# Kernel tuning notes

Measured on AMD Instinct MI355X. Metric: run time of the kernel, lower is better.

The kernel has to match this reference:

```python
import jax, jax.numpy as jnp
import numpy as np

EPS = 1e-6

def _feature(x):
    # phi(x) = concat(relu(x), relu(-x)) along the last dim: (b,h,n,d) -> (b,h,n,2d)
    return jnp.concatenate([jax.nn.relu(x), jax.nn.relu(-x)], axis=-1)

def setup_inputs() -> dict:
    key = jax.random.key(0)
    kq, kk, kv = jax.random.split(key, 3)
    shape = (4, 16, 8192, 64)  # (batch, heads, seq_len, dim)
    Q = jax.random.normal(kq, shape, dtype=jnp.float32)
    K = jax.random.normal(kk, shape, dtype=jnp.float32)
    V = jax.random.normal(kv, shape, dtype=jnp.float32)
    return {"Q": Q, "K": K, "V": V}

def reference(Q, K, V):
    Qf = _feature(Q)  # (b,h,n,2d)
    Kf = _feature(K)  # (b,h,n,2d)
    # KV outer-product reduction over sequence: (b,h,2d,m)
    KV = jnp.einsum('bhnd,bhnm->bhdm', Kf, V)
    out = jnp.einsum('bhnd,bhdm->bhnm', Qf, KV)  # (b,h,n,m)
    K_sum = Kf.sum(axis=2)  # (b,h,2d)
    normalizer = jnp.einsum('bhnd,bhd->bhn', Qf, K_sum)  # (b,h,n)
    return out / (normalizer[..., None] + EPS)
```

## Files before the change

kernel.cpp:

```cpp
#include <hip/hip_runtime.h>

typedef __bf16 bf16x8 __attribute__((ext_vector_type(8)));
typedef __bf16 bf16x4 __attribute__((ext_vector_type(4)));
typedef float f32x4 __attribute__((ext_vector_type(4)));

#define BH_TOT 64
#define SEQ 8192
#define DIM 64
#define NCH 16
#define CHN (SEQ / NCH)
#define KV_STRIDE 68
#define KV_ROWS 128

__global__ __launch_bounds__(256) void fla_ph1(const float* __restrict__ K,
                                               const float* __restrict__ V,
                                               float* __restrict__ kvf) {
  const int blk = blockIdx.x;
  const int bh = blk / NCH;
  const int ch = blk % NCH;
  const float* Kp = K + (size_t)bh * SEQ * DIM + (size_t)ch * CHN * DIM;
  const float* Vp = V + (size_t)bh * SEQ * DIM + (size_t)ch * CHN * DIM;

  __shared__ __bf16 Kb[32][68];
  __shared__ __bf16 Vb[32][68];

  const int tid = threadIdx.x;
  const int lane = tid & 63;
  const int w = tid >> 6;
  const int quad = lane >> 4;
  const int col = lane & 15;

  f32x4 acc[2][5];
#pragma unroll
  for (int mt = 0; mt < 2; ++mt)
#pragma unroll
    for (int nt = 0; nt < 5; ++nt)
      acc[mt][nt] = (f32x4){0.f, 0.f, 0.f, 0.f};

  bf16x8 bones;
#pragma unroll
  for (int j = 0; j < 8; ++j) bones[j] = (__bf16)0.f;
  if (col == 0) {
#pragma unroll
    for (int j = 0; j < 8; ++j) bones[j] = (__bf16)1.0f;
  }

  const int fcol0 = ((w & 1) << 5) + col;
  const bool neg = (w >= 2);

  for (int s = 0; s < CHN / 32; ++s) {
    const float* Ks = Kp + s * 32 * DIM;
    const float* Vs = Vp + s * 32 * DIM;
    __syncthreads();
#pragma unroll
    for (int i = 0; i < 2; ++i) {
      int idx = tid + i * 256;
      int r = idx >> 4;
      int c4 = (idx & 15) << 2;
      float4 kk = *(const float4*)(Ks + r * DIM + c4);
      float4 vv = *(const float4*)(Vs + r * DIM + c4);
      bf16x4 kb4, vb4;
      kb4[0] = (__bf16)kk.x; kb4[1] = (__bf16)kk.y;
      kb4[2] = (__bf16)kk.z; kb4[3] = (__bf16)kk.w;
      vb4[0] = (__bf16)vv.x; vb4[1] = (__bf16)vv.y;
      vb4[2] = (__bf16)vv.z; vb4[3] = (__bf16)vv.w;
      *(bf16x4*)&Kb[r][c4] = kb4;
      *(bf16x4*)&Vb[r][c4] = vb4;
    }
    __syncthreads();

    bf16x8 a0, a1, bfr[5];
#pragma unroll
    for (int j = 0; j < 8; ++j) {
      int rr = quad * 8 + j;
      float k0 = (float)Kb[rr][fcol0];
      float k1 = (float)Kb[rr][fcol0 + 16];
      if (neg) { k0 = -k0; k1 = -k1; }
      a0[j] = (__bf16)fmaxf(k0, 0.f);
      a1[j] = (__bf16)fmaxf(k1, 0.f);
      bfr[0][j] = Vb[rr][col];
      bfr[1][j] = Vb[rr][col + 16];
      bfr[2][j] = Vb[rr][col + 32];
      bfr[3][j] = Vb[rr][col + 48];
    }
    bfr[4] = bones;
#pragma unroll
    for (int nt = 0; nt < 5; ++nt) {
      acc[0][nt] = __builtin_amdgcn_mfma_f32_16x16x32_bf16(a0, bfr[nt], acc[0][nt], 0, 0, 0);
      acc[1][nt] = __builtin_amdgcn_mfma_f32_16x16x32_bf16(a1, bfr[nt], acc[1][nt], 0, 0, 0);
    }
  }

  float* dst = kvf + (size_t)bh * KV_ROWS * KV_STRIDE;
#pragma unroll
  for (int mt = 0; mt < 2; ++mt) {
    int feat = (w * 2 + mt) * 16 + quad * 4;
#pragma unroll
    for (int nt = 0; nt < 5; ++nt) {
      int c = nt * 16 + col;
      if (c <= 64) {
#pragma unroll
        for (int r = 0; r < 4; ++r)
          atomicAdd(&dst[(size_t)(feat + r) * KV_STRIDE + c], acc[mt][nt][r]);
      }
    }
  }
}

__global__ __launch_bounds__(256) void fla_ph2(const float* __restrict__ Q,
                                               const float* __restrict__ kvf,
                                               float* __restrict__ out) {
  const int blk = blockIdx.x;
  const int bh = blk >> 5;
  const int rb = blk & 31;
  const float* Qp = Q + (size_t)bh * SEQ * DIM + (size_t)rb * 256 * DIM;
  float* Op = out + (size_t)bh * SEQ * DIM + (size_t)rb * 256 * DIM;

  __shared__ __bf16 kvb[128][66];
  const float* src = kvf + (size_t)bh * KV_ROWS * KV_STRIDE;
  for (int i = threadIdx.x; i < 128 * 66; i += 256) {
    int k = i / 66;
    int c = i - k * 66;
    float v = (c <= 64) ? src[(size_t)k * KV_STRIDE + c] : 0.f;
    kvb[k][c] = (__bf16)v;
  }
  __syncthreads();

  const int lane = threadIdx.x & 63;
  const int w = threadIdx.x >> 6;
  const int quad = lane >> 4;
  const int col = lane & 15;

  bf16x8 bfr[4][5];
#pragma unroll
  for (int kt = 0; kt < 4; ++kt) {
#pragma unroll
    for (int j = 0; j < 8; ++j) {
      int k = kt * 32 + quad * 8 + j;
      bfr[kt][0][j] = kvb[k][col];
      bfr[kt][1][j] = kvb[k][col + 16];
      bfr[kt][2][j] = kvb[k][col + 32];
      bfr[kt][3][j] = kvb[k][col + 48];
      bfr[kt][4][j] = (col == 0) ? kvb[k][64] : (__bf16)0.f;
    }
  }

#pragma unroll
  for (int mt = 0; mt < 4; ++mt) {
    const float* qrow = Qp + (size_t)(w * 64 + mt * 16 + col) * DIM;
    float4 q0 = *(const float4*)(qrow + quad * 8);
    float4 q1 = *(const float4*)(qrow + quad * 8 + 4);
    float4 q2 = *(const float4*)(qrow + 32 + quad * 8);
    float4 q3 = *(const float4*)(qrow + 32 + quad * 8 + 4);
    float qv[16];
    *(float4*)&qv[0] = q0;  *(float4*)&qv[4] = q1;
    *(float4*)&qv[8] = q2;  *(float4*)&qv[12] = q3;
    bf16x8 a0, a1, a2, a3;
#pragma unroll
    for (int j = 0; j < 8; ++j) {
      a0[j] = (__bf16)fmaxf(qv[j], 0.f);
      a2[j] = (__bf16)fmaxf(-qv[j], 0.f);
      a1[j] = (__bf16)fmaxf(qv[8 + j], 0.f);
      a3[j] = (__bf16)fmaxf(-qv[8 + j], 0.f);
    }
    f32x4 acc[5];
#pragma unroll
    for (int nt = 0; nt < 5; ++nt) acc[nt] = (f32x4){0.f, 0.f, 0.f, 0.f};
#pragma unroll
    for (int nt = 0; nt < 5; ++nt) {
      acc[nt] = __builtin_amdgcn_mfma_f32_16x16x32_bf16(a0, bfr[0][nt], acc[nt], 0, 0, 0);
      acc[nt] = __builtin_amdgcn_mfma_f32_16x16x32_bf16(a1, bfr[1][nt], acc[nt], 0, 0, 0);
      acc[nt] = __builtin_amdgcn_mfma_f32_16x16x32_bf16(a2, bfr[2][nt], acc[nt], 0, 0, 0);
      acc[nt] = __builtin_amdgcn_mfma_f32_16x16x32_bf16(a3, bfr[3][nt], acc[nt], 0, 0, 0);
    }
    float inv[4];
#pragma unroll
    for (int r = 0; r < 4; ++r) {
      float nrm = __shfl((float)acc[4][r], lane & 48, 64);
      inv[r] = 1.0f / (nrm + 1e-6f);
    }
    float* orow = Op + (size_t)(w * 64 + mt * 16) * DIM;
#pragma unroll
    for (int nt = 0; nt < 4; ++nt)
#pragma unroll
      for (int r = 0; r < 4; ++r)
        orow[(size_t)(quad * 4 + r) * DIM + nt * 16 + col] = acc[nt][r] * inv[r];
  }
}

extern "C" void kernel_launch(void* const* d_in, const int* in_sizes, int n_in,
                              void* d_out, int out_size, void* d_ws, size_t ws_size,
                              hipStream_t stream) {
  const float* Q = (const float*)d_in[0];
  const float* K = (const float*)d_in[1];
  const float* V = (const float*)d_in[2];
  float* out = (float*)d_out;
  float* kvf = (float*)d_ws;

  hipMemsetAsync(kvf, 0, (size_t)BH_TOT * KV_ROWS * KV_STRIDE * sizeof(float), stream);
  fla_ph1<<<dim3(BH_TOT * NCH), dim3(256), 0, stream>>>(K, V, kvf);
  fla_ph2<<<dim3(BH_TOT * 32), dim3(256), 0, stream>>>(Q, kvf, out);
}
```

Measured before the change: 474.8 us.

## Prefetch K/V registers and use 512-thread blocks in phase-one reduction

Phase one now runs 512 threads per block with 8 waves, each owning one 16-feature tile instead of two, and stages 64 rows per iteration. Global loads for the next tile are issued into registers before the LDS store and barrier of the current tile, so memory latency overlaps the MFMA work. The launch bound asks for higher occupancy. In exchange, each wave re-reads V fragments from LDS for both row slices, and the atomic output layout is remapped to the new wave-to-feature assignment.

Result: faster. 457.5 us (-3.7%).

```diff
diff --git a/kernel.cpp b/kernel.cpp
--- a/kernel.cpp
+++ b/kernel.cpp
@@ -9,20 +9,22 @@
 #define DIM 64
 #define NCH 16
 #define CHN (SEQ / NCH)
+#define ROWS 64
+#define NR (CHN / ROWS)
 #define KV_STRIDE 68
 #define KV_ROWS 128
 
-__global__ __launch_bounds__(256) void fla_ph1(const float* __restrict__ K,
-                                               const float* __restrict__ V,
-                                               float* __restrict__ kvf) {
+__global__ __launch_bounds__(512, 8) void fla_ph1(const float* __restrict__ K,
+                                                  const float* __restrict__ V,
+                                                  float* __restrict__ kvf) {
   const int blk = blockIdx.x;
   const int bh = blk / NCH;
   const int ch = blk % NCH;
   const float* Kp = K + (size_t)bh * SEQ * DIM + (size_t)ch * CHN * DIM;
   const float* Vp = V + (size_t)bh * SEQ * DIM + (size_t)ch * CHN * DIM;
 
-  __shared__ __bf16 Kb[32][68];
-  __shared__ __bf16 Vb[32][68];
+  __shared__ __bf16 Kb[ROWS][68];
+  __shared__ __bf16 Vb[ROWS][68];
 
   const int tid = threadIdx.x;
   const int lane = tid & 63;
@@ -30,12 +32,14 @@
   const int quad = lane >> 4;
   const int col = lane & 15;
 
-  f32x4 acc[2][5];
-#pragma unroll
-  for (int mt = 0; mt < 2; ++mt)
-#pragma unroll
-    for (int nt = 0; nt < 5; ++nt)
-      acc[mt][nt] = (f32x4){0.f, 0.f, 0.f, 0.f};
+  const int r0 = tid >> 4;
+  const int c0 = (tid & 15) << 2;
+  const int off0 = r0 * DIM + c0;
+  const int off1 = off0 + 32 * DIM;
+
+  f32x4 acc[5];
+#pragma unroll
+  for (int nt = 0; nt < 5; ++nt) acc[nt] = (f32x4){0.f, 0.f, 0.f, 0.f};
 
   bf16x8 bones;
 #pragma unroll
@@ -45,64 +49,68 @@
     for (int j = 0; j < 8; ++j) bones[j] = (__bf16)1.0f;
   }
 
-  const int fcol0 = ((w & 1) << 5) + col;
-  const bool neg = (w >= 2);
-
-  for (int s = 0; s < CHN / 32; ++s) {
-    const float* Ks = Kp + s * 32 * DIM;
-    const float* Vs = Vp + s * 32 * DIM;
+  const int kcol = ((w & 3) << 4) + col;
+  const bool neg = (w >= 4);
+
+  float4 pk0 = *(const float4*)(Kp + off0);
+  float4 pk1 = *(const float4*)(Kp + off1);
+  float4 pv0 = *(const float4*)(Vp + off0);
+  float4 pv1 = *(const float4*)(Vp + off1);
+
+  for (int s = 0; s < NR; ++s) {
+    bf16x4 kb0, kb1, vb0, vb1;
+    kb0[0] = (__bf16)pk0.x; kb0[1] = (__bf16)pk0.y; kb0[2] = (__bf16)pk0.z; kb0[3] = (__bf16)pk0.w;
+    kb1[0] = (__bf16)pk1.x; kb1[1] = (__bf16)pk1.y; kb1[2] = (__bf16)pk1.z; kb1[3] = (__bf16)pk1.w;
+    vb0[0] = (__bf16)pv0.x; vb0[1] = (__bf16)pv0.y; vb0[2] = (__bf16)pv0.z; vb0[3] = (__bf16)pv0.w;
+    vb1[0] = (__bf16)pv1.x; vb1[1] = (__bf16)pv1.y; vb1[2] = (__bf16)pv1.z; vb1[3] = (__bf16)pv1.w;
+
+    if (s + 1 < NR) {
+      const float* Kn = Kp + (s + 1) * ROWS * DIM;
+      const float* Vn = Vp + (s + 1) * ROWS * DIM;
+      pk0 = *(const float4*)(Kn + off0);
+      pk1 = *(const float4*)(Kn + off1);
+      pv0 = *(const float4*)(Vn + off0);
+      pv1 = *(const float4*)(Vn + off1);
+    }
+
     __syncthreads();
-#pragma unroll
-    for (int i = 0; i < 2; ++i) {
-      int idx = tid + i * 256;
-      int r = idx >> 4;
-      int c4 = (idx & 15) << 2;
-      float4 kk = *(const float4*)(Ks + r * DIM + c4);
-      float4 vv = *(const float4*)(Vs + r * DIM + c4);
-      bf16x4 kb4, vb4;
-      kb4[0] = (__bf16)kk.x; kb4[1] = (__bf16)kk.y;
-      kb4[2] = (__bf16)kk.z; kb4[3] = (__bf16)kk.w;
-      vb4[0] = (__bf16)vv.x; vb4[1] = (__bf16)vv.y;
-      vb4[2] = (__bf16)vv.z; vb4[3] = (__bf16)vv.w;
-      *(bf16x4*)&Kb[r][c4] = kb4;
-      *(bf16x4*)&Vb[r][c4] = vb4;
-    }
+    *(bf16x4*)&Kb[r0][c0]      = kb0;
+    *(bf16x4*)&Kb[r0 + 32][c0] = kb1;
+    *(bf16x4*)&Vb[r0][c0]      = vb0;
+    *(bf16x4*)&Vb[r0 + 32][c0] = vb1;
     __syncthreads();
 
-    bf16x8 a0, a1, bfr[5];
-#pragma unroll
-    for (int j = 0; j < 8; ++j) {
-      int rr = quad * 8 + j;
-      float k0 = (float)Kb[rr][fcol0];
-      float k1 = (float)Kb[rr][fcol0 + 16];
-      if (neg) { k0 = -k0; k1 = -k1; }
-      a0[j] = (__bf16)fmaxf(k0, 0.f);
-      a1[j] = (__bf16)fmaxf(k1, 0.f);
-      bfr[0][j] = Vb[rr][col];
-      bfr[1][j] = Vb[rr][col + 16];
-      bfr[2][j] = Vb[rr][col + 32];
-      bfr[3][j] = Vb[rr][col + 48];
-    }
-    bfr[4] = bones;
-#pragma unroll
-    for (int nt = 0; nt < 5; ++nt) {
-      acc[0][nt] = __builtin_amdgcn_mfma_f32_16x16x32_bf16(a0, bfr[nt], acc[0][nt], 0, 0, 0);
-      acc[1][nt] = __builtin_amdgcn_mfma_f32_16x16x32_bf16(a1, bfr[nt], acc[1][nt], 0, 0, 0);
+#pragma unroll
+    for (int sl = 0; sl < 2; ++sl) {
+      bf16x8 a;
+#pragma unroll
+      for (int j = 0; j < 8; ++j) {
+        int rr = sl * 32 + quad * 8 + j;
+        float kv = (float)Kb[rr][kcol];
+        if (neg) kv = -kv;
+        a[j] = (__bf16)fmaxf(kv, 0.f);
+      }
+#pragma unroll
+      for (int nt = 0; nt < 4; ++nt) {
+        bf16x8 b;
+#pragma unroll
+        for (int j = 0; j < 8; ++j)
+          b[j] = Vb[sl * 32 + quad * 8 + j][col + nt * 16];
+        acc[nt] = __builtin_amdgcn_mfma_f32_16x16x32_bf16(a, b, acc[nt], 0, 0, 0);
+      }
+      acc[4] = __builtin_amdgcn_mfma_f32_16x16x32_bf16(a, bones, acc[4], 0, 0, 0);
     }
   }
 
   float* dst = kvf + (size_t)bh * KV_ROWS * KV_STRIDE;
-#pragma unroll
-  for (int mt = 0; mt < 2; ++mt) {
-    int feat = (w * 2 + mt) * 16 + quad * 4;
-#pragma unroll
-    for (int nt = 0; nt < 5; ++nt) {
-      int c = nt * 16 + col;
-      if (c <= 64) {
-#pragma unroll
-        for (int r = 0; r < 4; ++r)
-          atomicAdd(&dst[(size_t)(feat + r) * KV_STRIDE + c], acc[mt][nt][r]);
-      }
+  const int feat = w * 16 + quad * 4;
+#pragma unroll
+  for (int nt = 0; nt < 5; ++nt) {
+    int c = nt * 16 + col;
+    if (c <= 64) {
+#pragma unroll
+      for (int r = 0; r < 4; ++r)
+        atomicAdd(&dst[(size_t)(feat + r) * KV_STRIDE + c], acc[nt][r]);
     }
   }
 }
@@ -198,6 +206,6 @@
   float* kvf = (float*)d_ws;
 
   hipMemsetAsync(kvf, 0, (size_t)BH_TOT * KV_ROWS * KV_STRIDE * sizeof(float), stream);
-  fla_ph1<<<dim3(BH_TOT * NCH), dim3(256), 0, stream>>>(K, V, kvf);
+  fla_ph1<<<dim3(BH_TOT * NCH), dim3(512), 0, stream>>>(K, V, kvf);
   fla_ph2<<<dim3(BH_TOT * 32), dim3(256), 0, stream>>>(Q, kvf, out);
 }
```
